# Kernel optimization log

Measured on AMD Instinct MI355X. Metric: run time of the kernel, lower is better.

Reference implementation:

```python
import jax, jax.numpy as jnp
import numpy as np

N_HEADS = 16
KQ_DIM = 64
EMB_DIM = 1024
CTX_DIM = 1024
EPS = 1e-5

def _layernorm(x, w, b):
    # LayerNorm over last dim (kq_dim), elementwise affine
    mu = jnp.mean(x, axis=-1, keepdims=True)
    var = jnp.mean(jnp.square(x - mu), axis=-1, keepdims=True)
    return (x - mu) * jax.lax.rsqrt(var + EPS) * w + b

def setup_inputs() -> dict:
    key = jax.random.key(0)
    ks = jax.random.split(key, 10)
    B, SQ, SK = 2, 2048, 2048
    inner = N_HEADS * KQ_DIM
    s_e = 1.0 / np.sqrt(EMB_DIM)
    s_c = 1.0 / np.sqrt(CTX_DIM)
    s_i = 1.0 / np.sqrt(inner)
    return {
        "emb": jax.random.normal(ks[0], (B, SQ, EMB_DIM), jnp.float32),
        "context": jax.random.normal(ks[1], (B, SK, CTX_DIM), jnp.float32),
        "Wq": jax.random.uniform(ks[2], (inner, EMB_DIM), jnp.float32, -s_e, s_e),
        "Wk": jax.random.uniform(ks[3], (inner, CTX_DIM), jnp.float32, -s_c, s_c),
        "Wv": jax.random.uniform(ks[4], (inner, CTX_DIM), jnp.float32, -s_c, s_c),
        "Wu": jax.random.uniform(ks[5], (EMB_DIM, inner), jnp.float32, -s_i, s_i),
        "bu": jax.random.uniform(ks[6], (EMB_DIM,), jnp.float32, -s_i, s_i),
        "qn_w": jnp.ones((KQ_DIM,), jnp.float32),
        "qn_b": jnp.zeros((KQ_DIM,), jnp.float32),
        "kn_w": jnp.ones((KQ_DIM,), jnp.float32),
        "kn_b": jnp.zeros((KQ_DIM,), jnp.float32),
    }

def reference(emb, context, Wq, Wk, Wv, Wu, bu, qn_w, qn_b, kn_w, kn_b):
    B, SQ, _ = emb.shape
    SK = context.shape[1]
    # projections (no bias), reshape to [B, H, S, D]
    q = (emb @ Wq.T).reshape(B, SQ, N_HEADS, KQ_DIM).transpose(0, 2, 1, 3)
    k = (context @ Wk.T).reshape(B, SK, N_HEADS, KQ_DIM).transpose(0, 2, 1, 3)
    v = (context @ Wv.T).reshape(B, SK, N_HEADS, KQ_DIM).transpose(0, 2, 1, 3)
    q = _layernorm(q, qn_w, qn_b)
    k = _layernorm(k, kn_w, kn_b)
    scale = 1.0 / jnp.sqrt(jnp.asarray(KQ_DIM, emb.dtype))
    attn = jnp.einsum('bhqd,bhkd->bhqk', q, k) * scale
    attn = jax.nn.softmax(attn, axis=-1)
    out = jnp.einsum('bhqk,bhkd->bhqd', attn, v)
    out = out.transpose(0, 2, 1, 3).reshape(B, SQ, N_HEADS * KQ_DIM)
    return out @ Wu.T + bu
```

## Files before the change

kernel.cpp:

```cpp
#include <hip/hip_runtime.h>


typedef __attribute__((ext_vector_type(8)))  short bf16x8;
typedef __attribute__((ext_vector_type(4)))  short bf16x4;
typedef __attribute__((ext_vector_type(4)))  float f32x4;
typedef __attribute__((ext_vector_type(16))) float f32x16;
typedef __attribute__((ext_vector_type(4)))  unsigned int u32x4;

#define SM_SCALE 0.18033688f

typedef __attribute__((address_space(1))) const void cg_void;
typedef __attribute__((address_space(3))) void lds_void_t;

__device__ __forceinline__ void gl_lds16(const void* g, void* l){
  __builtin_amdgcn_global_load_lds((cg_void*)g, (lds_void_t*)l, 16, 0, 0);
}

__device__ __forceinline__ short f2b(float f){
  unsigned int u;
  __builtin_memcpy(&u, &f, 4);
  u += 0x7fffu + ((u >> 16) & 1u);
  return (short)(u >> 16);
}

__global__ __launch_bounds__(256) void cvt6_kernel(
    const float* __restrict__ emb, const float* __restrict__ ctx,
    const float* __restrict__ Wq, const float* __restrict__ Wk,
    const float* __restrict__ Wv, const float* __restrict__ Wu,
    short* __restrict__ o_emb, short* __restrict__ o_ctx,
    short* __restrict__ o_wq, short* __restrict__ o_wk,
    short* __restrict__ o_wv, short* __restrict__ o_wu)
{
  const long M1 = 1024L * 1024L, M4 = 4L * M1;
  long e = ((long)blockIdx.x * 256 + threadIdx.x) * 4;
  if (e >= 12L * M1) return;
  const float* src; short* dst; long off;
  if      (e <     M4)      { src = emb; dst = o_emb; off = e;           }
  else if (e < 2 * M4)      { src = ctx; dst = o_ctx; off = e - M4;      }
  else if (e < 2 * M4 + M1) { src = Wq;  dst = o_wq;  off = e - 2 * M4;  }
  else if (e < 2 * M4 + 2*M1){src = Wk;  dst = o_wk;  off = e - 2*M4 - M1;}
  else if (e < 2 * M4 + 3*M1){src = Wv;  dst = o_wv;  off = e - 2*M4 - 2*M1;}
  else                      { src = Wu;  dst = o_wu;  off = e - 2*M4 - 3*M1;}
  f32x4 v = *(const f32x4*)(src + off);
  bf16x4 o;
  o[0] = f2b(v[0]); o[1] = f2b(v[1]); o[2] = f2b(v[2]); o[3] = f2b(v[3]);
  *(bf16x4*)(dst + off) = o;
}

__global__ __launch_bounds__(256, 3) void gemm_qkv_kernel(
    const short* __restrict__ embh, const short* __restrict__ ctxh,
    const short* __restrict__ Wqh, const short* __restrict__ Wkh,
    const short* __restrict__ Wvh,
    short* __restrict__ qo, short* __restrict__ ko, short* __restrict__ vto,
    const float* __restrict__ qw, const float* __restrict__ qb,
    const float* __restrict__ kw, const float* __restrict__ kb)
{
  const int K = 1024;
  __shared__ short As[128 * 64];
  __shared__ short Bs[128 * 64];
  const int tid  = threadIdx.x;
  const int wave = tid >> 6, lane = tid & 63;
  const int quad = lane >> 4, r16 = lane & 15;
  const int wm = (wave >> 1) * 64, wn = (wave & 1) * 64;

  const int task = blockIdx.y;
  int bn, bm, N;
  const short *A, *B;
  if (task == 2){
    bn = (blockIdx.x & 31) * 128; bm = (blockIdx.x >> 5) * 128; N = 4096;
    A = Wvh; B = ctxh;
  } else {
    bm = (blockIdx.x & 31) * 128; bn = (blockIdx.x >> 5) * 128; N = 1024;
    A = task ? ctxh : embh; B = task ? Wkh : Wqh;
  }

  f32x4 acc[4][4];
#pragma unroll
  for (int i = 0; i < 4; i++)
#pragma unroll
    for (int j = 0; j < 4; j++)
      acc[i][j] = (f32x4){0.f, 0.f, 0.f, 0.f};

  const int sr7 = (lane >> 3) & 7;
  const size_t arow = (size_t)(bm + wave * 8 + (lane >> 3)) * K
                      + (((lane & 7) ^ sr7) * 8);
  const size_t brow = (size_t)(bn + wave * 8 + (lane >> 3)) * K
                      + (((lane & 7) ^ sr7) * 8);
  const int sw = ((quad ^ (r16 & 7)) << 3);

  for (int k0 = 0; k0 < K; k0 += 64){
#pragma unroll
    for (int i = 0; i < 4; i++)
      gl_lds16(A + arow + (size_t)32 * i * K + k0, &As[wave * 512 + i * 2048]);
#pragma unroll
    for (int i = 0; i < 4; i++)
      gl_lds16(B + brow + (size_t)32 * i * K + k0, &Bs[wave * 512 + i * 2048]);
    __syncthreads();
#pragma unroll
    for (int kk = 0; kk < 2; kk++){
      const int off = sw ^ (kk << 5);
      bf16x8 af[4], bq[4];
#pragma unroll
      for (int i = 0; i < 4; i++)
        af[i] = *(const bf16x8*)(&As[(wm + i*16 + r16) * 64 + off]);
#pragma unroll
      for (int j = 0; j < 4; j++)
        bq[j] = *(const bf16x8*)(&Bs[(wn + j*16 + r16) * 64 + off]);
#pragma unroll
      for (int i = 0; i < 4; i++)
#pragma unroll
        for (int j = 0; j < 4; j++)
          acc[i][j] = __builtin_amdgcn_mfma_f32_16x16x32_bf16(af[i], bq[j], acc[i][j], 0, 0, 0);
    }
    __syncthreads();
  }

  if (task < 2){
    short* Ch = task ? ko : qo;
    const float* lw = task ? kw : qw;
    const float* lb = task ? kb : qb;
    const float post = task ? 1.0f : SM_SCALE;
    float wv[4], bv[4];
#pragma unroll
    for (int j = 0; j < 4; j++){
      wv[j] = lw[j*16 + r16] * post;
      bv[j] = lb[j*16 + r16] * post;
    }
#pragma unroll
    for (int i = 0; i < 4; i++){
#pragma unroll
      for (int t = 0; t < 4; t++){
        float a[4];
#pragma unroll
        for (int j = 0; j < 4; j++) a[j] = acc[i][j][t];
        float s = a[0] + a[1] + a[2] + a[3];
        s += __shfl_xor(s, 1); s += __shfl_xor(s, 2);
        s += __shfl_xor(s, 4); s += __shfl_xor(s, 8);
        const float mu = s * 0.015625f;
        float d[4], sq = 0.f;
#pragma unroll
        for (int j = 0; j < 4; j++){ d[j] = a[j] - mu; sq += d[j]*d[j]; }
        sq += __shfl_xor(sq, 1); sq += __shfl_xor(sq, 2);
        sq += __shfl_xor(sq, 4); sq += __shfl_xor(sq, 8);
        const float si = rsqrtf(sq * 0.015625f + 1e-5f);
        const size_t row = (size_t)(bm + wm + i*16 + quad*4 + t);
#pragma unroll
        for (int j = 0; j < 4; j++)
          Ch[row * 1024 + (bn + wn + j*16 + r16)] = f2b(d[j] * si * wv[j] + bv[j]);
      }
    }
  } else {
#pragma unroll
    for (int i = 0; i < 4; i++){
#pragma unroll
      for (int j = 0; j < 4; j++){
        const int p = (r16 & 3) | ((j & 1) << 2) | (((r16 >> 2) & 1) << 3)
                      | (((r16 >> 3) & 1) << 4);
        const int col = ((bn + wn + j*16 + r16) & ~31) | p;
#pragma unroll
        for (int t = 0; t < 4; t++){
          const size_t row = (size_t)(bm + wm + i*16 + quad*4 + t);
          vto[row * (size_t)N + col] = f2b(acc[i][j][t]);
        }
      }
    }
  }
}

__global__ __launch_bounds__(256, 4) void gemm_out_kernel(
    const short* __restrict__ A, const short* __restrict__ B,
    float* __restrict__ Cf, const float* __restrict__ bias)
{
  const int K = 1024, N = 1024;
  __shared__ short As[64 * 64];
  __shared__ short Bs[64 * 64];
  const int tid  = threadIdx.x;
  const int wave = tid >> 6, lane = tid & 63;
  const int quad = lane >> 4, r16 = lane & 15;
  const int wm = (wave >> 1) * 32, wn = (wave & 1) * 32;
  const int bm = blockIdx.x * 64, bn = blockIdx.y * 64;

  f32x4 acc[2][2];
#pragma unroll
  for (int i = 0; i < 2; i++)
#pragma unroll
    for (int j = 0; j < 2; j++)
      acc[i][j] = (f32x4){0.f, 0.f, 0.f, 0.f};

  const int sr7 = (lane >> 3) & 7;
  const size_t arow = (size_t)(bm + wave * 8 + (lane >> 3)) * K
                      + (((lane & 7) ^ sr7) * 8);
  const size_t brow = (size_t)(bn + wave * 8 + (lane >> 3)) * K
                      + (((lane & 7) ^ sr7) * 8);
  const int sw = ((quad ^ (r16 & 7)) << 3);

  for (int k0 = 0; k0 < K; k0 += 64){
#pragma unroll
    for (int i = 0; i < 2; i++){
      gl_lds16(A + arow + (size_t)32 * i * K + k0, &As[wave * 512 + i * 2048]);
      gl_lds16(B + brow + (size_t)32 * i * K + k0, &Bs[wave * 512 + i * 2048]);
    }
    __syncthreads();
#pragma unroll
    for (int kk = 0; kk < 2; kk++){
      const int off = sw ^ (kk << 5);
      bf16x8 af[2], bq[2];
#pragma unroll
      for (int i = 0; i < 2; i++)
        af[i] = *(const bf16x8*)(&As[(wm + i*16 + r16) * 64 + off]);
#pragma unroll
      for (int j = 0; j < 2; j++)
        bq[j] = *(const bf16x8*)(&Bs[(wn + j*16 + r16) * 64 + off]);
#pragma unroll
      for (int i = 0; i < 2; i++)
#pragma unroll
        for (int j = 0; j < 2; j++)
          acc[i][j] = __builtin_amdgcn_mfma_f32_16x16x32_bf16(af[i], bq[j], acc[i][j], 0, 0, 0);
    }
    __syncthreads();
  }

#pragma unroll
  for (int i = 0; i < 2; i++){
#pragma unroll
    for (int j = 0; j < 2; j++){
      const int col = bn + wn + j*16 + r16;
#pragma unroll
      for (int t = 0; t < 4; t++){
        const size_t row = (size_t)(bm + wm + i*16 + quad*4 + t);
        Cf[row * N + col] = acc[i][j][t] + bias[col];
      }
    }
  }
}

__global__ __launch_bounds__(512, 4) void flash2_kernel(
    const short* __restrict__ Q, const short* __restrict__ K,
    const short* __restrict__ Vt, short* __restrict__ O)
{
  __shared__ __align__(16) long long smem8[8192];
  short* Ks  = (short*)smem8;
  short* Vts = Ks + 16384;
  float* scr = (float*)smem8;

  const int tid = threadIdx.x;
  const int wave = tid >> 6, lane = tid & 63;
  const int half = wave >> 2, wg = wave & 3;
  const int hh = lane >> 5, q5 = lane & 31;
  const int h = blockIdx.x, qb = blockIdx.y, b = blockIdx.z;
  const int q0 = qb * 128 + wg * 32;

  const size_t kbase = ((size_t)b * 2048) * 1024 + (size_t)h * 64;
  const size_t vbase = ((size_t)h * 64) * 4096 + (size_t)b * 2048;

  bf16x8 qf[4];
  {
    const size_t qrow = ((size_t)b * 2048 + q0 + q5) * 1024 + (size_t)h * 64;
#pragma unroll
    for (int c = 0; c < 4; c++)
      qf[c] = *(const bf16x8*)(Q + qrow + c * 16 + hh * 8);
  }

  bf16x8 onesf;
#pragma unroll
  for (int j = 0; j < 8; j++) onesf[j] = (short)0x3F80;

  f32x16 oacc[2], oaccl;
#pragma unroll
  for (int t = 0; t < 16; t++){ oacc[0][t] = 0.f; oacc[1][t] = 0.f; oaccl[t] = 0.f; }

  const int srow = lane >> 3;
  const int csrc = ((lane & 7) ^ srow) * 8;
  const int wr0 = wg * 16;

#define STAGE(bufi, kt)                                                         \
  {                                                                             \
    const short* ks = K + kbase + (size_t)((kt) * 64 + wr0 + srow) * 1024 + csrc; \
    const short* vs = Vt + vbase + (size_t)(wr0 + srow) * 4096 + (kt) * 64 + csrc; \
    short* kd = Ks  + (half * 2 + (bufi)) * 4096 + wr0 * 64;                    \
    short* vd = Vts + (half * 2 + (bufi)) * 4096 + wr0 * 64;                    \
    gl_lds16(ks,            kd);                                                \
    gl_lds16(ks + 8 * 1024, kd + 512);                                          \
    gl_lds16(vs,            vd);                                                \
    gl_lds16(vs + 8 * 4096, vd + 512);                                          \
  }

  STAGE(0, half)

  for (int i = 0; i < 16; i++){
    const int buf = i & 1;
    __syncthreads();
    if (i + 1 < 16) STAGE(buf ^ 1, 2 * (i + 1) + half)

    const short* kb_l = Ks  + (half * 2 + buf) * 4096;
    const short* vb_l = Vts + (half * 2 + buf) * 4096;

    bf16x8 kf[2][4];
#pragma unroll
    for (int s32 = 0; s32 < 2; s32++){
      const int key = s32 * 32 + q5;
#pragma unroll
      for (int c = 0; c < 4; c++)
        kf[s32][c] = *(const bf16x8*)(&kb_l[key * 64 + (((2*c + hh) ^ (key & 7)) << 3)]);
    }
    f32x16 sacc[2];
#pragma unroll
    for (int t = 0; t < 16; t++){ sacc[0][t] = 0.f; sacc[1][t] = 0.f; }
#pragma unroll
    for (int c = 0; c < 4; c++){
      sacc[0] = __builtin_amdgcn_mfma_f32_32x32x16_bf16(kf[0][c], qf[c], sacc[0], 0, 0, 0);
      sacc[1] = __builtin_amdgcn_mfma_f32_32x32x16_bf16(kf[1][c], qf[c], sacc[1], 0, 0, 0);
    }

#pragma unroll
    for (int s32 = 0; s32 < 2; s32++){
      unsigned int pu[16];
#pragma unroll
      for (int t = 0; t < 16; t++){
        const float e = __builtin_amdgcn_exp2f(sacc[s32][t]);
        unsigned int u; __builtin_memcpy(&u, &e, 4);
        pu[t] = u + 0x8000u;
      }

#pragma unroll
      for (int c = 0; c < 2; c++){
        u32x4 tmp;
        tmp[0] = __builtin_amdgcn_perm(pu[4*c + 1], pu[4*c + 0], 0x07060302u);
        tmp[1] = __builtin_amdgcn_perm(pu[4*c + 3], pu[4*c + 2], 0x07060302u);
        tmp[2] = __builtin_amdgcn_perm(pu[8 + 4*c + 1], pu[8 + 4*c + 0], 0x07060302u);
        tmp[3] = __builtin_amdgcn_perm(pu[8 + 4*c + 3], pu[8 + 4*c + 2], 0x07060302u);
        bf16x8 pf; __builtin_memcpy(&pf, &tmp, 16);
#pragma unroll
        for (int mt = 0; mt < 2; mt++){
          const int d = mt * 32 + q5;
          bf16x8 vf = *(const bf16x8*)(&vb_l[d * 64 + (((s32*4 + 2*c + hh) ^ (d & 7)) << 3)]);
          oacc[mt] = __builtin_amdgcn_mfma_f32_32x32x16_bf16(vf, pf, oacc[mt], 0, 0, 0);
        }
        oaccl = __builtin_amdgcn_mfma_f32_32x32x16_bf16(onesf, pf, oaccl, 0, 0, 0);
      }
    }
  }

  const float lhalf = oaccl[0];
  __syncthreads();
  float* base = scr + (wg * 64 + lane) * 33;
  if (half == 1){
#pragma unroll
    for (int t = 0; t < 16; t++){ base[t] = oacc[0][t]; base[16 + t] = oacc[1][t]; }
    scr[8448 + wg * 64 + lane] = lhalf;
  }
  __syncthreads();
  if (half == 0){
    const float l2 = scr[8448 + wg * 64 + lane];
    const float linv = 1.0f / (lhalf + l2);
    const size_t orow = ((size_t)b * 2048 + q0 + q5) * 1024 + (size_t)h * 64;
#pragma unroll
    for (int mt = 0; mt < 2; mt++){
#pragma unroll
      for (int g = 0; g < 4; g++){
        bf16x4 o4;
#pragma unroll
        for (int u = 0; u < 4; u++)
          o4[u] = f2b((oacc[mt][g*4 + u] + base[mt*16 + g*4 + u]) * linv);
        *(bf16x4*)(O + orow + mt*32 + g*8 + 4*hh) = o4;
      }
    }
  }
}
#undef STAGE

extern "C" void kernel_launch(void* const* d_in, const int* in_sizes, int n_in,
                              void* d_out, int out_size, void* d_ws, size_t ws_size,
                              hipStream_t stream) {
  const float* emb  = (const float*)d_in[0];
  const float* ctx  = (const float*)d_in[1];
  const float* Wq   = (const float*)d_in[2];
  const float* Wk   = (const float*)d_in[3];
  const float* Wv   = (const float*)d_in[4];
  const float* Wu   = (const float*)d_in[5];
  const float* bu   = (const float*)d_in[6];
  const float* qn_w = (const float*)d_in[7];
  const float* qn_b = (const float*)d_in[8];
  const float* kn_w = (const float*)d_in[9];
  const float* kn_b = (const float*)d_in[10];
  float* out = (float*)d_out;

  const size_t BIG = (size_t)4096 * 1024;
  const size_t WSZ = (size_t)1024 * 1024;
  short* ws   = (short*)d_ws;
  short* embh = ws;
  short* ctxh = embh + BIG;
  short* Wqh  = ctxh + BIG;
  short* Wkh  = Wqh + WSZ;
  short* Wvh  = Wkh + WSZ;
  short* Wuh  = Wvh + WSZ;
  short* qh   = Wuh + WSZ;
  short* kh   = qh + BIG;
  short* vth  = kh + BIG;
  short* aoh  = vth + BIG;

  cvt6_kernel<<<12288, 256, 0, stream>>>(emb, ctx, Wq, Wk, Wv, Wu,
                                         embh, ctxh, Wqh, Wkh, Wvh, Wuh);

  gemm_qkv_kernel<<<dim3(256, 3), 256, 0, stream>>>(
      embh, ctxh, Wqh, Wkh, Wvh, qh, kh, vth,
      qn_w, qn_b, kn_w, kn_b);

  flash2_kernel<<<dim3(16, 16, 2), 512, 0, stream>>>(qh, kh, vth, aoh);

  gemm_out_kernel<<<dim3(64, 16), 256, 0, stream>>>(aoh, Wuh, out, bu);
}
```

Baseline: 193.5 us.

## Process two query tiles per wave in flash kernel, drop ones-MFMA row sum

The attention kernel now uses 256-thread blocks where each wave handles 64 query rows (two 32-row groups), so each K/V fragment read from LDS feeds twice as many MFMAs. The row-sum of probabilities is computed with scalar adds plus a cross-half shuffle instead of an extra MFMA against a ones vector. Each thread issues more global-to-LDS loads per stage, and the final cross-half reduction runs in two passes through shared scratch. In exchange the kernel uses more registers and has fewer waves per block, which may reduce occupancy and latency hiding.

```diff
diff --git a/kernel.cpp b/kernel.cpp
--- a/kernel.cpp
+++ b/kernel.cpp
@@ -234,7 +234,7 @@
   }
 }
 
-__global__ __launch_bounds__(512, 4) void flash2_kernel(
+__global__ __launch_bounds__(256, 2) void flash2_kernel(
     const short* __restrict__ Q, const short* __restrict__ K,
     const short* __restrict__ Vt, short* __restrict__ O)
 {
@@ -245,33 +245,34 @@
 
   const int tid = threadIdx.x;
   const int wave = tid >> 6, lane = tid & 63;
-  const int half = wave >> 2, wg = wave & 3;
+  const int half = wave >> 1, wg = wave & 1;
   const int hh = lane >> 5, q5 = lane & 31;
   const int h = blockIdx.x, qb = blockIdx.y, b = blockIdx.z;
-  const int q0 = qb * 128 + wg * 32;
+  const int q0 = qb * 128 + wg * 64;
 
   const size_t kbase = ((size_t)b * 2048) * 1024 + (size_t)h * 64;
   const size_t vbase = ((size_t)h * 64) * 4096 + (size_t)b * 2048;
 
-  bf16x8 qf[4];
-  {
-    const size_t qrow = ((size_t)b * 2048 + q0 + q5) * 1024 + (size_t)h * 64;
+  bf16x8 qf[2][4];
+#pragma unroll
+  for (int qg = 0; qg < 2; qg++){
+    const size_t qrow = ((size_t)b * 2048 + q0 + qg * 32 + q5) * 1024 + (size_t)h * 64;
 #pragma unroll
     for (int c = 0; c < 4; c++)
-      qf[c] = *(const bf16x8*)(Q + qrow + c * 16 + hh * 8);
-  }
-
-  bf16x8 onesf;
-#pragma unroll
-  for (int j = 0; j < 8; j++) onesf[j] = (short)0x3F80;
-
-  f32x16 oacc[2], oaccl;
-#pragma unroll
-  for (int t = 0; t < 16; t++){ oacc[0][t] = 0.f; oacc[1][t] = 0.f; oaccl[t] = 0.f; }
+      qf[qg][c] = *(const bf16x8*)(Q + qrow + c * 16 + hh * 8);
+  }
+
+  f32x16 oacc[2][2];
+#pragma unroll
+  for (int t = 0; t < 16; t++){
+    oacc[0][0][t] = 0.f; oacc[0][1][t] = 0.f;
+    oacc[1][0][t] = 0.f; oacc[1][1][t] = 0.f;
+  }
+  float lacc[2] = {0.f, 0.f};
 
   const int srow = lane >> 3;
   const int csrc = ((lane & 7) ^ srow) * 8;
-  const int wr0 = wg * 16;
+  const int wr0 = wg * 32;
 
 #define STAGE(bufi, kt)                                                         \
   {                                                                             \
@@ -279,10 +280,14 @@
     const short* vs = Vt + vbase + (size_t)(wr0 + srow) * 4096 + (kt) * 64 + csrc; \
     short* kd = Ks  + (half * 2 + (bufi)) * 4096 + wr0 * 64;                    \
     short* vd = Vts + (half * 2 + (bufi)) * 4096 + wr0 * 64;                    \
-    gl_lds16(ks,            kd);                                                \
-    gl_lds16(ks + 8 * 1024, kd + 512);                                          \
-    gl_lds16(vs,            vd);                                                \
-    gl_lds16(vs + 8 * 4096, vd + 512);                                          \
+    gl_lds16(ks,             kd);                                               \
+    gl_lds16(ks +  8 * 1024, kd + 512);                                         \
+    gl_lds16(ks + 16 * 1024, kd + 1024);                                        \
+    gl_lds16(ks + 24 * 1024, kd + 1536);                                        \
+    gl_lds16(vs,             vd);                                               \
+    gl_lds16(vs +  8 * 4096, vd + 512);                                         \
+    gl_lds16(vs + 16 * 4096, vd + 1024);                                        \
+    gl_lds16(vs + 24 * 4096, vd + 1536);                                        \
   }
 
   STAGE(0, half)
@@ -303,68 +308,93 @@
       for (int c = 0; c < 4; c++)
         kf[s32][c] = *(const bf16x8*)(&kb_l[key * 64 + (((2*c + hh) ^ (key & 7)) << 3)]);
     }
-    f32x16 sacc[2];
-#pragma unroll
-    for (int t = 0; t < 16; t++){ sacc[0][t] = 0.f; sacc[1][t] = 0.f; }
+
+    f32x16 sacc[2][2];
+#pragma unroll
+    for (int t = 0; t < 16; t++){
+      sacc[0][0][t] = 0.f; sacc[0][1][t] = 0.f;
+      sacc[1][0][t] = 0.f; sacc[1][1][t] = 0.f;
+    }
 #pragma unroll
     for (int c = 0; c < 4; c++){
-      sacc[0] = __builtin_amdgcn_mfma_f32_32x32x16_bf16(kf[0][c], qf[c], sacc[0], 0, 0, 0);
-      sacc[1] = __builtin_amdgcn_mfma_f32_32x32x16_bf16(kf[1][c], qf[c], sacc[1], 0, 0, 0);
+      sacc[0][0] = __builtin_amdgcn_mfma_f32_32x32x16_bf16(kf[0][c], qf[0][c], sacc[0][0], 0, 0, 0);
+      sacc[0][1] = __builtin_amdgcn_mfma_f32_32x32x16_bf16(kf[1][c], qf[0][c], sacc[0][1], 0, 0, 0);
+      sacc[1][0] = __builtin_amdgcn_mfma_f32_32x32x16_bf16(kf[0][c], qf[1][c], sacc[1][0], 0, 0, 0);
+      sacc[1][1] = __builtin_amdgcn_mfma_f32_32x32x16_bf16(kf[1][c], qf[1][c], sacc[1][1], 0, 0, 0);
+    }
+
+    bf16x8 pf[2][2][2];
+#pragma unroll
+    for (int qg = 0; qg < 2; qg++){
+#pragma unroll
+      for (int s32 = 0; s32 < 2; s32++){
+        unsigned int pu[16];
+        float pp[4] = {0.f, 0.f, 0.f, 0.f};
+#pragma unroll
+        for (int t = 0; t < 16; t++){
+          const float e = __builtin_amdgcn_exp2f(sacc[qg][s32][t]);
+          pp[t & 3] += e;
+          unsigned int u; __builtin_memcpy(&u, &e, 4);
+          pu[t] = u + 0x8000u;
+        }
+        lacc[qg] += (pp[0] + pp[1]) + (pp[2] + pp[3]);
+#pragma unroll
+        for (int c = 0; c < 2; c++){
+          u32x4 tmp;
+          tmp[0] = __builtin_amdgcn_perm(pu[4*c + 1], pu[4*c + 0], 0x07060302u);
+          tmp[1] = __builtin_amdgcn_perm(pu[4*c + 3], pu[4*c + 2], 0x07060302u);
+          tmp[2] = __builtin_amdgcn_perm(pu[8 + 4*c + 1], pu[8 + 4*c + 0], 0x07060302u);
+          tmp[3] = __builtin_amdgcn_perm(pu[8 + 4*c + 3], pu[8 + 4*c + 2], 0x07060302u);
+          __builtin_memcpy(&pf[qg][s32][c], &tmp, 16);
+        }
+      }
     }
 
 #pragma unroll
     for (int s32 = 0; s32 < 2; s32++){
-      unsigned int pu[16];
-#pragma unroll
-      for (int t = 0; t < 16; t++){
-        const float e = __builtin_amdgcn_exp2f(sacc[s32][t]);
-        unsigned int u; __builtin_memcpy(&u, &e, 4);
-        pu[t] = u + 0x8000u;
-      }
-
 #pragma unroll
       for (int c = 0; c < 2; c++){
-        u32x4 tmp;
-        tmp[0] = __builtin_amdgcn_perm(pu[4*c + 1], pu[4*c + 0], 0x07060302u);
-        tmp[1] = __builtin_amdgcn_perm(pu[4*c + 3], pu[4*c + 2], 0x07060302u);
-        tmp[2] = __builtin_amdgcn_perm(pu[8 + 4*c + 1], pu[8 + 4*c + 0], 0x07060302u);
-        tmp[3] = __builtin_amdgcn_perm(pu[8 + 4*c + 3], pu[8 + 4*c + 2], 0x07060302u);
-        bf16x8 pf; __builtin_memcpy(&pf, &tmp, 16);
 #pragma unroll
         for (int mt = 0; mt < 2; mt++){
           const int d = mt * 32 + q5;
           bf16x8 vf = *(const bf16x8*)(&vb_l[d * 64 + (((s32*4 + 2*c + hh) ^ (d & 7)) << 3)]);
-          oacc[mt] = __builtin_amdgcn_mfma_f32_32x32x16_bf16(vf, pf, oacc[mt], 0, 0, 0);
+          oacc[0][mt] = __builtin_amdgcn_mfma_f32_32x32x16_bf16(vf, pf[0][s32][c], oacc[0][mt], 0, 0, 0);
+          oacc[1][mt] = __builtin_amdgcn_mfma_f32_32x32x16_bf16(vf, pf[1][s32][c], oacc[1][mt], 0, 0, 0);
         }
-        oaccl = __builtin_amdgcn_mfma_f32_32x32x16_bf16(onesf, pf, oaccl, 0, 0, 0);
-      }
-    }
-  }
-
-  const float lhalf = oaccl[0];
+      }
+    }
+  }
+
+  const int widx = wg * 64 + lane;
   __syncthreads();
-  float* base = scr + (wg * 64 + lane) * 33;
-  if (half == 1){
-#pragma unroll
-    for (int t = 0; t < 16; t++){ base[t] = oacc[0][t]; base[16 + t] = oacc[1][t]; }
-    scr[8448 + wg * 64 + lane] = lhalf;
-  }
-  __syncthreads();
-  if (half == 0){
-    const float l2 = scr[8448 + wg * 64 + lane];
-    const float linv = 1.0f / (lhalf + l2);
-    const size_t orow = ((size_t)b * 2048 + q0 + q5) * 1024 + (size_t)h * 64;
-#pragma unroll
-    for (int mt = 0; mt < 2; mt++){
-#pragma unroll
-      for (int g = 0; g < 4; g++){
-        bf16x4 o4;
-#pragma unroll
-        for (int u = 0; u < 4; u++)
-          o4[u] = f2b((oacc[mt][g*4 + u] + base[mt*16 + g*4 + u]) * linv);
-        *(bf16x4*)(O + orow + mt*32 + g*8 + 4*hh) = o4;
-      }
-    }
+#pragma unroll
+  for (int qg = 0; qg < 2; qg++){
+    const float lh = lacc[qg] + __shfl_xor(lacc[qg], 32);
+    if (half == 1){
+      float* base = scr + widx * 33;
+#pragma unroll
+      for (int t = 0; t < 16; t++){ base[t] = oacc[qg][0][t]; base[16 + t] = oacc[qg][1][t]; }
+      scr[4224 + widx] = lh;
+    }
+    __syncthreads();
+    if (half == 0){
+      const float* base = scr + widx * 33;
+      const float l2 = scr[4224 + widx];
+      const float linv = 1.0f / (lh + l2);
+      const size_t orow = ((size_t)b * 2048 + q0 + qg * 32 + q5) * 1024 + (size_t)h * 64;
+#pragma unroll
+      for (int mt = 0; mt < 2; mt++){
+#pragma unroll
+        for (int g = 0; g < 4; g++){
+          bf16x4 o4;
+#pragma unroll
+          for (int u = 0; u < 4; u++)
+            o4[u] = f2b((oacc[qg][mt][g*4 + u] + base[mt*16 + g*4 + u]) * linv);
+          *(bf16x4*)(O + orow + mt*32 + g*8 + 4*hh) = o4;
+        }
+      }
+    }
+    __syncthreads();
   }
 }
 #undef STAGE
@@ -406,7 +436,7 @@
       embh, ctxh, Wqh, Wkh, Wvh, qh, kh, vth,
       qn_w, qn_b, kn_w, kn_b);
 
-  flash2_kernel<<<dim3(16, 16, 2), 512, 0, stream>>>(qh, kh, vth, aoh);
+  flash2_kernel<<<dim3(16, 16, 2), 256, 0, stream>>>(qh, kh, vth, aoh);
 
   gemm_out_kernel<<<dim3(64, 16), 256, 0, stream>>>(aoh, Wuh, out, bu);
 }
```

After: 190.8 us. No clear change (-1.4%).
